# Optimization experiments

Hardware: AMD Instinct MI355X
Metric: run time of the kernel (lower is better)

The kernel has to match this reference:

```python
import jax, jax.numpy as jnp
from jax import lax
import numpy as np

DN = ('NCHW', 'OIHW', 'NCHW')

def _bn(x, g, b):
    # BatchNorm2d in training mode: batch statistics, biased variance, eps=1e-5
    m = jnp.mean(x, axis=(0, 2, 3), keepdims=True)
    v = jnp.var(x, axis=(0, 2, 3), keepdims=True)
    return g[None, :, None, None] * (x - m) * lax.rsqrt(v + 1e-5) + b[None, :, None, None]

def _conv(x, w, b, s, p):
    y = lax.conv_general_dilated(x, w, (s, s), [(p, p), (p, p)], dimension_numbers=DN)
    return y + b[None, :, None, None]

def _convt(x, w, b, s, p):
    # torch ConvTranspose2d weight layout [in, out, k, k]; equivalent to
    # input-dilated conv with flipped, transposed kernel and padding k-1-p.
    k = w.shape[2]
    pp = k - 1 - p
    w2 = jnp.flip(w, (2, 3)).transpose(1, 0, 2, 3)  # [out, in, k, k]
    y = lax.conv_general_dilated(x, w2, (1, 1), [(pp, pp), (pp, pp)],
                                 lhs_dilation=(s, s), dimension_numbers=DN)
    return y + b[None, :, None, None]

def setup_inputs() -> dict:
    key = jax.random.key(0)
    ks = jax.random.split(key, 16)
    f32 = jnp.float32
    def rn(i, shape, s):
        return jax.random.normal(ks[i], shape, f32) * s
    K = 256
    inp = {
        'x': jax.random.normal(ks[0], (128, 3, 64, 64), f32),
        'codebook': jax.random.uniform(ks[1], (256, 256), f32, -1.0 / K, 1.0 / K),
        'e_w1': rn(2, (64, 3, 3, 3), 0.19), 'e_b1': jnp.zeros((64,), f32),
        'e_g1': jnp.ones((64,), f32), 'e_be1': jnp.zeros((64,), f32),
        'e_w2': rn(3, (128, 64, 4, 4), 0.031), 'e_b2': jnp.zeros((128,), f32),
        'e_g2': jnp.ones((128,), f32), 'e_be2': jnp.zeros((128,), f32),
        'e_w3': rn(4, (192, 128, 4, 4), 0.022), 'e_b3': jnp.zeros((192,), f32),
        'e_g3': jnp.ones((192,), f32), 'e_be3': jnp.zeros((192,), f32),
        'e_w4': rn(5, (256, 192, 1, 1), 0.072), 'e_b4': jnp.zeros((256,), f32),
        'd_w1': rn(6, (256, 192, 1, 1), 0.062), 'd_b1': jnp.zeros((192,), f32),
        'd_g1': jnp.ones((192,), f32), 'd_be1': jnp.zeros((192,), f32),
        'd_w2': rn(7, (192, 128, 4, 4), 0.018), 'd_b2': jnp.zeros((128,), f32),
        'd_g2': jnp.ones((128,), f32), 'd_be2': jnp.zeros((128,), f32),
        'd_w3': rn(8, (128, 64, 4, 4), 0.022), 'd_b3': jnp.zeros((64,), f32),
        'd_g3': jnp.ones((64,), f32), 'd_be3': jnp.zeros((64,), f32),
        'd_w4': rn(9, (3, 64, 3, 3), 0.042), 'd_b4': jnp.zeros((3,), f32),
    }
    return inp

def reference(x, codebook,
              e_w1, e_b1, e_g1, e_be1, e_w2, e_b2, e_g2, e_be2,
              e_w3, e_b3, e_g3, e_be3, e_w4, e_b4,
              d_w1, d_b1, d_g1, d_be1, d_w2, d_b2, d_g2, d_be2,
              d_w3, d_b3, d_g3, d_be3, d_w4, d_b4):
    # encoder
    h = jax.nn.relu(_bn(_conv(x, e_w1, e_b1, 1, 1), e_g1, e_be1))
    h = jax.nn.relu(_bn(_conv(h, e_w2, e_b2, 2, 1), e_g2, e_be2))
    h = jax.nn.relu(_bn(_conv(h, e_w3, e_b3, 2, 1), e_g3, e_be3))
    h = _conv(h, e_w4, e_b4, 1, 0)  # [B, 256, 16, 16]
    B, C, H, W = h.shape
    Z = h.transpose(0, 2, 3, 1).reshape(-1, C)  # [N, D]
    # fused cdist via ||a||^2 + ||b||^2 - 2ab (argmin invariant to const offsets)
    d2 = (jnp.sum(Z * Z, axis=1, keepdims=True)
          + jnp.sum(codebook * codebook, axis=1)[None, :]
          - 2.0 * (Z @ codebook.T))  # [N, K]
    j = jnp.argmin(d2, axis=1)
    Wj = codebook[j]  # [N, D]
    loss_commit = jnp.mean(jnp.sum((Z - lax.stop_gradient(Wj)) ** 2, axis=1))
    loss_code = jnp.mean(jnp.sum((lax.stop_gradient(Z) - Wj) ** 2, axis=1))
    hq = Wj.reshape(B, H, W, C).transpose(0, 3, 1, 2)
    # decoder
    g = jax.nn.relu(_bn(_convt(hq, d_w1, d_b1, 1, 0), d_g1, d_be1))
    g = jax.nn.relu(_bn(_convt(g, d_w2, d_b2, 2, 1), d_g2, d_be2))
    g = jax.nn.relu(_bn(_convt(g, d_w3, d_b3, 2, 1), d_g3, d_be3))
    g = _conv(g, d_w4, d_b4, 1, 1)  # [B, 3, 64, 64]
    return g, loss_commit, loss_code
```

## Files before the change

kernel.cpp:

```cpp
#include <hip/hip_runtime.h>

#define TPB 256

typedef __attribute__((ext_vector_type(4))) float v4f;
typedef __attribute__((ext_vector_type(8))) short v8s;

__device__ __forceinline__ float us2f(unsigned int u) {
    union { unsigned int i; float f; } w; w.i = u << 16; return w.f;
}
__device__ __forceinline__ unsigned short f2us(float f) {
    union { float ff; unsigned int i; } w; w.ff = f;
    unsigned int u = w.i;
    return (unsigned short)((u + 0x7fffu + ((u >> 16) & 1u)) >> 16);
}
__device__ __forceinline__ void gl_lds16(const unsigned short* g, unsigned short* l) {
    __builtin_amdgcn_global_load_lds(
        (const __attribute__((address_space(1))) unsigned int*)g,
        (__attribute__((address_space(3))) unsigned int*)l, 16, 0, 0);
}

__global__ __launch_bounds__(TPB) void repack_all(
    const float* __restrict__ e_w1, const float* __restrict__ d_w4,
    const float* __restrict__ e_w2, const float* __restrict__ e_w3,
    const float* __restrict__ e_w4, const float* __restrict__ d_w1,
    const float* __restrict__ d_w2, const float* __restrict__ d_w3,
    unsigned short* __restrict__ we1, unsigned short* __restrict__ wd4r,
    unsigned short* __restrict__ we2, unsigned short* __restrict__ we3,
    unsigned short* __restrict__ we4, unsigned short* __restrict__ wd1,
    unsigned short* __restrict__ wd2, unsigned short* __restrict__ wd3,
    unsigned short* __restrict__ zpage)
{
    int gid = blockIdx.x * TPB + threadIdx.x;
    if (gid < 2048) {
        int idx = gid;
        int k = idx & 31, co = idx >> 5;
        we1[idx] = (k < 27) ? f2us(e_w1[co * 27 + k]) : (unsigned short)0;
        return;
    }
    gid -= 2048;
    if (gid < 9216) {
        int idx = gid;
        int e = idx & 7;
        int lane = (idx >> 3) & 63;
        int kk = idx >> 9;
        int lr = lane & 15, lc = lane >> 4;
        int tap = kk >> 1, half = kk & 1;
        int ci = half * 32 + lc * 8 + e;
        wd4r[idx] = (lr < 3) ? f2us(d_w4[((size_t)lr * 64 + ci) * 9 + tap])
                             : (unsigned short)0;
        return;
    }
    gid -= 9216;
    if (gid < 131072) {
        int idx = gid;
        int e = idx & 7;
        int lane = (idx >> 3) & 63;
        int seg8 = (idx >> 9) & 7;
        int u = idx >> 12;
        int cb = u % 2, tap = u / 2;
        int lr = lane & 15, lc = lane >> 4;
        int kc = seg8 >> 2, sg = seg8 & 3;
        int co = cb * 64 + sg * 16 + lr;
        int ci = kc * 32 + lc * 8 + e;
        we2[idx] = f2us(e_w2[((size_t)co * 64 + ci) * 16 + tap]);
        return;
    }
    gid -= 131072;
    if (gid < 393216) {
        int idx = gid;
        int ci = idx % 128;
        int co = (idx / 128) % 192;
        int kk = idx / (128 * 192);
        we3[idx] = f2us(e_w3[((size_t)co * 128 + ci) * 16 + kk]);
        return;
    }
    gid -= 393216;
    if (gid < 49152) {
        int idx = gid;
        int ci = idx % 192;
        int co = (idx / 192) % 256;
        we4[idx] = f2us(e_w4[(size_t)co * 192 + ci]);
        return;
    }
    gid -= 49152;
    if (gid < 49152) {
        int idx = gid;
        int ci = idx % 256;
        int co = idx / 256;
        wd1[idx] = f2us(d_w1[(size_t)ci * 192 + co]);
        return;
    }
    gid -= 49152;
    if (gid < 393216) {
        int idx = gid;
        int e = idx & 7;
        int lane = (idx >> 3) & 63;
        int seg8 = (idx >> 9) & 7;
        int u = idx >> 12;
        int cb = u % 2;
        int u2 = u / 2;
        int cc = u2 % 3;
        int tk = u2 / 3;
        int kidx = tk & 3, cls = tk >> 2;
        int lr = lane & 15, lc = lane >> 4;
        int kc = seg8 >> 2, sg = seg8 & 3;
        int co = cb * 64 + sg * 16 + lr;
        int ci = cc * 64 + kc * 32 + lc * 8 + e;
        int ohp = cls >> 1, owp = cls & 1;
        int kh = ((ohp + 1) & 1) + 2 * (kidx >> 1);
        int kw = ((owp + 1) & 1) + 2 * (kidx & 1);
        wd2[idx] = f2us(d_w2[((size_t)ci * 128 + co) * 16 + kh * 4 + kw]);
        return;
    }
    gid -= 393216;
    if (gid < 131072) {
        int idx = gid;
        int e = idx & 7;
        int lane = (idx >> 3) & 63;
        int seg8 = (idx >> 9) & 7;
        int u2 = idx >> 12;
        int cc = u2 % 2;
        int tk = u2 / 2;
        int kidx = tk & 3, cls = tk >> 2;
        int lr = lane & 15, lc = lane >> 4;
        int kc = seg8 >> 2, sg = seg8 & 3;
        int co = sg * 16 + lr;
        int ci = cc * 64 + kc * 32 + lc * 8 + e;
        int ohp = cls >> 1, owp = cls & 1;
        int kh = ((ohp + 1) & 1) + 2 * (kidx >> 1);
        int kw = ((owp + 1) & 1) + 2 * (kidx & 1);
        wd3[idx] = f2us(d_w3[((size_t)ci * 64 + co) * 16 + kh * 4 + kw]);
        return;
    }
    gid -= 131072;
    if (gid < 128) zpage[gid] = 0;
}

__global__ __launch_bounds__(TPB) void e1_gemm(
    const float* __restrict__ x, const unsigned short* __restrict__ wrep,
    const float* __restrict__ bias, unsigned short* __restrict__ yout,
    float* __restrict__ part, int N)
{
    __shared__ __align__(16) unsigned short Ab[8 * 512];
    __shared__ __align__(16) unsigned short Bb[4 * 512];

    const int t = threadIdx.x, lane = t & 63, wave = t >> 6;
    const int wm = wave >> 1, wn = wave & 1;
    const int m0 = (int)blockIdx.x * 128;
    const int lr = lane & 15, lc = lane >> 4;

    gl_lds16(wrep + (size_t)(wave * 16 + lr) * 32 + lc * 8, &Bb[wave * 512]);

    {
        int r = m0 + (t >> 1);
        int h = t & 1;
        int n = r >> 12, oh = (r >> 6) & 63, ow = r & 63;
        unsigned short rowv[16];
#pragma unroll
        for (int kk = 0; kk < 16; kk++) {
            int k = h * 16 + kk;
            float v = 0.f;
            if (k < 27) {
                int ci = k / 9, tap = k % 9, kh = tap / 3, kw = tap % 3;
                int ih = oh - 1 + kh, iw = ow - 1 + kw;
                if ((unsigned)ih < 64u && (unsigned)iw < 64u)
                    v = x[(((size_t)n * 3 + ci) * 64 + ih) * 64 + iw];
            }
            rowv[kk] = f2us(v);
        }
        int rl = (t >> 1) & 15;
        int s = (t >> 1) >> 4;
        int base = s * 512 + (h * 32 + rl) * 8;
        *(int4*)&Ab[base] = *(const int4*)&rowv[0];
        *(int4*)&Ab[base + 128] = *(const int4*)&rowv[8];
    }
    __syncthreads();

    v4f acc[4][2];
#pragma unroll
    for (int i = 0; i < 4; i++)
#pragma unroll
        for (int j = 0; j < 2; j++)
#pragma unroll
            for (int r = 0; r < 4; r++) acc[i][j][r] = 0.f;

    v8s a[4], b[2];
#pragma unroll
    for (int i = 0; i < 4; i++)
        a[i] = *(const v8s*)&Ab[(wm * 4 + i) * 512 + lane * 8];
#pragma unroll
    for (int j = 0; j < 2; j++)
        b[j] = *(const v8s*)&Bb[(wn * 2 + j) * 512 + lane * 8];
#pragma unroll
    for (int i = 0; i < 4; i++)
#pragma unroll
        for (int j = 0; j < 2; j++)
            acc[i][j] = __builtin_amdgcn_mfma_f32_16x16x32_bf16(a[i], b[j], acc[i][j], 0, 0, 0);

    float sloc[2], qloc[2];
#pragma unroll
    for (int j = 0; j < 2; j++) { sloc[j] = 0.f; qloc[j] = 0.f; }

#pragma unroll
    for (int i = 0; i < 4; i++) {
        int mr = wm * 64 + i * 16 + (lane >> 4) * 4;
#pragma unroll
        for (int j = 0; j < 2; j++) {
            int col = wn * 32 + j * 16 + (lane & 15);
            float bs = bias[col];
#pragma unroll
            for (int r = 0; r < 4; r++) {
                int row = m0 + mr + r;
                int n = row >> 12, oh = (row >> 6) & 63, ow = row & 63;
                int cls = ((oh & 1) << 1) | (ow & 1);
                size_t crow = ((((size_t)cls * N + n) * 32 + (oh >> 1)) * 32 + (ow >> 1));
                float v = acc[i][j][r] + bs;
                yout[crow * 64 + col] = f2us(v);
                sloc[j] += v;
                qloc[j] += v * v;
            }
        }
    }

    __syncthreads();
    float* red = (float*)Ab;
    for (int i = t; i < 128; i += TPB) red[i] = 0.f;
    __syncthreads();
#pragma unroll
    for (int j = 0; j < 2; j++) {
        float s = sloc[j], qv = qloc[j];
        s += __shfl_xor(s, 16); s += __shfl_xor(s, 32);
        qv += __shfl_xor(qv, 16); qv += __shfl_xor(qv, 32);
        if ((lane >> 4) == 0) {
            int cl = wn * 32 + j * 16 + (lane & 15);
            atomicAdd(&red[cl], s);
            atomicAdd(&red[64 + cl], qv);
        }
    }
    __syncthreads();
    int PB = (int)gridDim.x, pb = (int)blockIdx.x;
    for (int i = t; i < 64; i += TPB) {
        part[(size_t)i * PB + pb] = red[i];
        part[(size_t)(64 + i) * PB + pb] = red[64 + i];
    }
}

template<int CIN, int COUT, int HO, int WO, int NCB>
__global__ __launch_bounds__(TPB) void conv_c(
    const unsigned short* __restrict__ xin, const unsigned short* __restrict__ wrep,
    const float* __restrict__ bias, unsigned short* __restrict__ yout,
    float* __restrict__ part, const unsigned short* __restrict__ zpage, int N)
{
    constexpr int NCI = CIN / 64;
    constexpr int NIT = 16 * NCI;
    __shared__ __align__(16) unsigned short Ab[2][16 * 1024];
    __shared__ __align__(16) unsigned short Bb[2][8 * 512];

    const int t = threadIdx.x, lane = t & 63, wave = t >> 6;
    int gdec = (int)blockIdx.x >> 3, xs = (int)blockIdx.x & 7;
    int cb = 0;
    if (NCB >= 2) { cb = gdec % NCB; gdec /= NCB; }
    const int tile = (gdec << 3) + xs;
    const int m0 = tile * 256;
    const int co0 = cb * 64;
    const int lr = lane & 15, lc = lane >> 4;

    const int jr7 = lane >> 3;
    const int sw = ((lane & 7) ^ jr7) * 8;

    int n_[4], oh_[4], ow0_[4];
#pragma unroll
    for (int q = 0; q < 4; q++) {
        int r0 = m0 + (wave * 4 + q) * 16;
        n_[q] = r0 / (HO * WO);
        int rem = r0 % (HO * WO);
        oh_[q] = rem / WO;
        ow0_[q] = rem % WO;
    }

    v4f acc[4][4];
#pragma unroll
    for (int i = 0; i < 4; i++)
#pragma unroll
        for (int j = 0; j < 4; j++)
#pragma unroll
            for (int r = 0; r < 4; r++) acc[i][j][r] = 0.f;

    auto stage = [&](int it, int buf) {
        const int tap = it / NCI, cc = it % NCI;
        const int kh = tap >> 2, kw = tap & 3;
        const int dcls = (((kh + 1) & 1) << 1) | ((kw + 1) & 1);
        const int dh2 = (kh - 1) >> 1;
        const int dw2 = (kw - 1) >> 1;
#pragma unroll
        for (int q = 0; q < 4; q++) {
            const int ih2 = oh_[q] + dh2;
            const bool ihv = (unsigned)ih2 < (unsigned)HO;
#pragma unroll
            for (int h = 0; h < 2; h++) {
                int iw2 = ow0_[q] + h * 8 + jr7 + dw2;
                bool av = ihv && (unsigned)iw2 < (unsigned)WO;
                size_t ab = ((((size_t)dcls * N + n_[q]) * HO + ih2) * WO + iw2) * CIN;
                const unsigned short* src = av ? xin + ab + cc * 64 + sw : zpage;
                gl_lds16(src, &Ab[buf][(wave * 4 + q) * 1024 + h * 512]);
            }
        }
        const unsigned short* wb = wrep
            + ((size_t)(tap * NCI + cc) * NCB + cb) * 4096;
        gl_lds16(wb + wave * 512 + lane * 8, &Bb[buf][wave * 512]);
        gl_lds16(wb + (4 + wave) * 512 + lane * 8, &Bb[buf][(4 + wave) * 512]);
    };

    auto compute = [&](int it, int buf) {
#pragma unroll
        for (int kc = 0; kc < 2; kc++) {
            v8s a[4], b[4];
#pragma unroll
            for (int i = 0; i < 4; i++)
                a[i] = *(const v8s*)&Ab[buf][(wave * 4 + i) * 1024 + lr * 64
                        + ((kc * 32 + lc * 8) ^ ((lr & 7) << 3))];
#pragma unroll
            for (int j = 0; j < 4; j++)
                b[j] = *(const v8s*)&Bb[buf][(kc * 4 + j) * 512 + lane * 8];
#pragma unroll
            for (int i = 0; i < 4; i++)
#pragma unroll
                for (int j = 0; j < 4; j++)
                    acc[i][j] = __builtin_amdgcn_mfma_f32_16x16x32_bf16(a[i], b[j], acc[i][j], 0, 0, 0);
        }
    };

    stage(0, 0);
    __syncthreads();

#pragma unroll
    for (int it = 0; it < NIT; ++it) {
        const int buf = it & 1;
        if (it + 1 < NIT) stage(it + 1, buf ^ 1);
        compute(it, buf);
        __syncthreads();
    }

    float sloc[4], qloc[4];
#pragma unroll
    for (int j = 0; j < 4; j++) { sloc[j] = 0.f; qloc[j] = 0.f; }

#pragma unroll
    for (int i = 0; i < 4; i++) {
        int mr = wave * 64 + i * 16 + (lane >> 4) * 4;
#pragma unroll
        for (int j = 0; j < 4; j++) {
            int col = co0 + j * 16 + (lane & 15);
            float bs = bias[col];
#pragma unroll
            for (int r = 0; r < 4; r++) {
                size_t gi = (size_t)(m0 + mr + r) * COUT + col;
                float v = acc[i][j][r] + bs;
                yout[gi] = f2us(v);
                sloc[j] += v;
                qloc[j] += v * v;
            }
        }
    }

    float* red = (float*)Ab;
    for (int i = t; i < 128; i += TPB) red[i] = 0.f;
    __syncthreads();
#pragma unroll
    for (int j = 0; j < 4; j++) {
        float s = sloc[j], qv = qloc[j];
        s += __shfl_xor(s, 16); s += __shfl_xor(s, 32);
        qv += __shfl_xor(qv, 16); qv += __shfl_xor(qv, 32);
        if ((lane >> 4) == 0) {
            int cl = j * 16 + (lane & 15);
            atomicAdd(&red[cl], s);
            atomicAdd(&red[64 + cl], qv);
        }
    }
    __syncthreads();
    const int TILES = (N * HO * WO) >> 8;
    const int pb = tile;
    for (int i = t; i < 64; i += TPB) {
        part[(size_t)(co0 + i) * TILES + pb] = red[i];
        part[(size_t)(COUT + co0 + i) * TILES + pb] = red[64 + i];
    }
}

template<int CIN, int COUT, int HIN, int WIN, int K, int S, int P, int BN,
         int OUTM, int NYB>
__global__ __launch_bounds__(TPB) void conv_mfma(
    const unsigned short* __restrict__ xin, const unsigned short* __restrict__ wrep,
    const float* __restrict__ bias, void* __restrict__ yout, void* __restrict__ yout2,
    float* __restrict__ part, const unsigned short* __restrict__ zpage, int N)
{
    constexpr int HOUT = (HIN + 2 * P - K) / S + 1;
    constexpr int WOUT = (WIN + 2 * P - K) / S + 1;
    constexpr int RN = BN / 32;
    constexpr int BSEG = BN / 16;
    constexpr int NCI = CIN / 64;
    constexpr int NIT = K * K * NCI;
    __shared__ __align__(16) unsigned short Ab[2][16 * 512];
    __shared__ __align__(16) unsigned short Bb[2][2 * BSEG * 512];

    const int t = threadIdx.x, lane = t & 63, wave = t >> 6;
    const int wm = wave >> 1, wn = wave & 1;
    int m0, co0;
    if (NYB == 2) {
        int g = (int)blockIdx.x >> 3, xs = (int)blockIdx.x & 7;
        co0 = (g & 1) * BN;
        m0 = (((g >> 1) << 3) + xs) * 128;
    } else {
        m0 = (int)blockIdx.x * 128;
        co0 = 0;
    }
    const int lr = lane & 15, lc = lane >> 4;

    int n_[2], oh_[2], ow_[2];
#pragma unroll
    for (int i = 0; i < 2; i++) {
        int r = m0 + (wave + 4 * i) * 16 + lr;
        n_[i] = r / (HOUT * WOUT);
        int rem = r % (HOUT * WOUT);
        oh_[i] = rem / WOUT;
        ow_[i] = rem % WOUT;
    }

    v4f acc[4][RN];
#pragma unroll
    for (int i = 0; i < 4; i++)
#pragma unroll
        for (int j = 0; j < RN; j++)
#pragma unroll
            for (int r = 0; r < 4; r++) acc[i][j][r] = 0.f;

    auto do_stage = [&](int it, int pb) {
        const int kk = it / NCI;
        const int ci0 = (it % NCI) * 64;
        const int kh = kk / K, kw = kk % K;
#pragma unroll
        for (int i = 0; i < 2; i++) {
            int ih = oh_[i] * S - P + kh;
            int iw = ow_[i] * S - P + kw;
            bool av = (unsigned)ih < (unsigned)HIN && (unsigned)iw < (unsigned)WIN;
            const unsigned short* b0 = av
                ? xin + (((size_t)n_[i] * HIN + ih) * WIN + iw) * CIN + lc * 8 + ci0
                : zpage;
            gl_lds16(b0, &Ab[pb][(wave + 4 * i) * 512]);
            gl_lds16(av ? b0 + 32 : zpage, &Ab[pb][(8 + wave + 4 * i) * 512]);
        }
        const unsigned short* wt = wrep + (size_t)kk * COUT * CIN;
#pragma unroll
        for (int i = 0; i < 2; i++) {
            int sgb = wave + 4 * i;
            if (sgb < BSEG) {
                const unsigned short* wb =
                    wt + (size_t)(co0 + sgb * 16 + lr) * CIN + ci0 + lc * 8;
                gl_lds16(wb, &Bb[pb][sgb * 512]);
                gl_lds16(wb + 32, &Bb[pb][(BSEG + sgb) * 512]);
            }
        }
    };

    do_stage(0, 0);
    __syncthreads();

    for (int it = 0; it < NIT; ++it) {
        const int pb = it & 1;
        if (it + 1 < NIT) do_stage(it + 1, pb ^ 1);

#pragma unroll
        for (int kc = 0; kc < 2; kc++) {
            v8s a[4], b[RN];
#pragma unroll
            for (int i = 0; i < 4; i++)
                a[i] = *(const v8s*)&Ab[pb][(kc * 8 + wm * 4 + i) * 512 + lane * 8];
#pragma unroll
            for (int j = 0; j < RN; j++)
                b[j] = *(const v8s*)&Bb[pb][(kc * BSEG + wn * RN + j) * 512 + lane * 8];
#pragma unroll
            for (int i = 0; i < 4; i++)
#pragma unroll
                for (int j = 0; j < RN; j++)
                    acc[i][j] = __builtin_amdgcn_mfma_f32_16x16x32_bf16(a[i], b[j], acc[i][j], 0, 0, 0);
        }
        __syncthreads();
    }

    float sloc[RN], qloc[RN];
#pragma unroll
    for (int j = 0; j < RN; j++) { sloc[j] = 0.f; qloc[j] = 0.f; }

#pragma unroll
    for (int i = 0; i < 4; i++) {
        int mr = wm * 64 + i * 16 + (lane >> 4) * 4;
#pragma unroll
        for (int j = 0; j < RN; j++) {
            int col = co0 + wn * (BN / 2) + j * 16 + (lane & 15);
            float bs = bias[col];
#pragma unroll
            for (int r = 0; r < 4; r++) {
                size_t g = (size_t)(m0 + mr + r) * COUT + col;
                float v = acc[i][j][r] + bs;
                if (OUTM == 2) {
                    unsigned short h = f2us(v);
                    ((unsigned short*)yout)[g] = h;
                    ((unsigned short*)yout2)[g] = f2us(v - us2f(h));
                } else {
                    ((unsigned short*)yout)[g] = f2us(v);
                    sloc[j] += v;
                    qloc[j] += v * v;
                }
            }
        }
    }

    if (OUTM == 0) {
        __syncthreads();
        float* red = (float*)Ab;
        for (int i = t; i < 2 * BN; i += TPB) red[i] = 0.f;
        __syncthreads();
#pragma unroll
        for (int j = 0; j < RN; j++) {
            float s = sloc[j], qv = qloc[j];
            s += __shfl_xor(s, 16); s += __shfl_xor(s, 32);
            qv += __shfl_xor(qv, 16); qv += __shfl_xor(qv, 32);
            if ((lane >> 4) == 0) {
                int cl = wn * (BN / 2) + j * 16 + (lane & 15);
                atomicAdd(&red[cl], s);
                atomicAdd(&red[BN + cl], qv);
            }
        }
        __syncthreads();
        int pb = (NYB == 2) ? (m0 >> 7) : (int)blockIdx.x;
        int PB = (NYB == 2) ? ((int)gridDim.x >> 1) : (int)gridDim.x;
        for (int i = t; i < BN; i += TPB) {
            int col = co0 + i;
            part[(size_t)col * PB + pb] = red[i];
            part[(size_t)(COUT + col) * PB + pb] = red[BN + i];
        }
    }
}

template<int CIN, int COUT, int HIN, int WIN, int NCB, int IN_CLS>
__global__ __launch_bounds__(TPB) void convt_c(
    const unsigned short* __restrict__ xin, const unsigned short* __restrict__ wrep,
    const float* __restrict__ bias, unsigned short* __restrict__ yout,
    float* __restrict__ part, const unsigned short* __restrict__ zpage, int N)
{
    constexpr int NCI = CIN / 64;
    constexpr int NIT = 4 * NCI;
    __shared__ __align__(16) unsigned short Ab[2][16 * 1024];
    __shared__ __align__(16) unsigned short Bb[2][8 * 512];

    const int t = threadIdx.x, lane = t & 63, wave = t >> 6;
    int gdec = (int)blockIdx.x >> 3, xs = (int)blockIdx.x & 7;
    int cb = 0;
    if (NCB == 2) { cb = gdec & 1; gdec >>= 1; }
    const int cls = gdec & 3;
    const int tile = ((gdec >> 2) << 3) + xs;
    const int m0 = tile * 256;
    const int co0 = cb * 64;
    const int ohp = cls >> 1, owp = cls & 1;
    const int khb = (ohp + 1) & 1, kwb = (owp + 1) & 1;
    const int dh0 = (ohp + 1 - khb) >> 1, dw0 = (owp + 1 - kwb) >> 1;
    const int lr = lane & 15, lc = lane >> 4;

    const int jr7 = lane >> 3;
    const int sw = ((lane & 7) ^ jr7) * 8;

    int n_[4], i_[4], j0_[4];
#pragma unroll
    for (int q = 0; q < 4; q++) {
        int r0 = m0 + (wave * 4 + q) * 16;
        n_[q] = r0 / (HIN * WIN);
        int rem = r0 % (HIN * WIN);
        i_[q] = rem / WIN;
        j0_[q] = rem % WIN;
    }

    v4f acc[4][4];
#pragma unroll
    for (int i = 0; i < 4; i++)
#pragma unroll
        for (int j = 0; j < 4; j++)
#pragma unroll
            for (int r = 0; r < 4; r++) acc[i][j][r] = 0.f;

    auto stage = [&](int it, int buf) {
        const int tap = it / NCI, cc = it % NCI;
        const int dh = dh0 - (tap >> 1);
        const int dw = dw0 - (tap & 1);
#pragma unroll
        for (int q = 0; q < 4; q++) {
            const int ih = i_[q] + dh;
            const bool ihv = (unsigned)ih < (unsigned)HIN;
#pragma unroll
            for (int h = 0; h < 2; h++) {
                int iw = j0_[q] + h * 8 + jr7 + dw;
                bool av = ihv && (unsigned)iw < (unsigned)WIN;
                size_t ab;
                if (IN_CLS) {
                    int clsi = ((ih & 1) << 1) | (iw & 1);
                    ab = ((((size_t)clsi * N + n_[q]) * (HIN / 2) + (ih >> 1)) * (WIN / 2)
                         + (iw >> 1)) * CIN;
                } else {
                    ab = (((size_t)n_[q] * HIN + ih) * WIN + iw) * CIN;
                }
                const unsigned short* src = av ? xin + ab + cc * 64 + sw : zpage;
                gl_lds16(src, &Ab[buf][(wave * 4 + q) * 1024 + h * 512]);
            }
        }
        const unsigned short* wb = wrep
            + ((size_t)((cls * 4 + tap) * NCI + cc) * NCB + cb) * 4096;
        gl_lds16(wb + wave * 512 + lane * 8, &Bb[buf][wave * 512]);
        gl_lds16(wb + (4 + wave) * 512 + lane * 8, &Bb[buf][(4 + wave) * 512]);
    };

    auto compute = [&](int it, int buf) {
#pragma unroll
        for (int kc = 0; kc < 2; kc++) {
            v8s a[4], b[4];
#pragma unroll
            for (int i = 0; i < 4; i++)
                a[i] = *(const v8s*)&Ab[buf][(wave * 4 + i) * 1024 + lr * 64
                        + ((kc * 32 + lc * 8) ^ ((lr & 7) << 3))];
#pragma unroll
            for (int j = 0; j < 4; j++)
                b[j] = *(const v8s*)&Bb[buf][(kc * 4 + j) * 512 + lane * 8];
#pragma unroll
            for (int i = 0; i < 4; i++)
#pragma unroll
                for (int j = 0; j < 4; j++)
                    acc[i][j] = __builtin_amdgcn_mfma_f32_16x16x32_bf16(a[i], b[j], acc[i][j], 0, 0, 0);
        }
    };

    stage(0, 0);
    __syncthreads();

#pragma unroll
    for (int it = 0; it < NIT; ++it) {
        const int buf = it & 1;
        if (it + 1 < NIT) stage(it + 1, buf ^ 1);
        compute(it, buf);
        __syncthreads();
    }

    float sloc[4], qloc[4];
#pragma unroll
    for (int j = 0; j < 4; j++) { sloc[j] = 0.f; qloc[j] = 0.f; }

    const size_t clsbase = (size_t)cls * N * HIN * WIN;
#pragma unroll
    for (int i = 0; i < 4; i++) {
        int mr = wave * 64 + i * 16 + (lane >> 4) * 4;
#pragma unroll
        for (int j = 0; j < 4; j++) {
            int col = co0 + j * 16 + (lane & 15);
            float bs = bias[col];
#pragma unroll
            for (int r = 0; r < 4; r++) {
                size_t gi = (clsbase + m0 + mr + r) * COUT + col;
                float v = acc[i][j][r] + bs;
                yout[gi] = f2us(v);
                sloc[j] += v;
                qloc[j] += v * v;
            }
        }
    }

    float* red = (float*)Ab;
    for (int i = t; i < 128; i += TPB) red[i] = 0.f;
    __syncthreads();
#pragma unroll
    for (int j = 0; j < 4; j++) {
        float s = sloc[j], qv = qloc[j];
        s += __shfl_xor(s, 16); s += __shfl_xor(s, 32);
        qv += __shfl_xor(qv, 16); qv += __shfl_xor(qv, 32);
        if ((lane >> 4) == 0) {
            int cl = j * 16 + (lane & 15);
            atomicAdd(&red[cl], s);
            atomicAdd(&red[64 + cl], qv);
        }
    }
    __syncthreads();
    const int TILES = (N * HIN * WIN) >> 8;
    const int PB = 4 * TILES;
    const int pb = cls * TILES + tile;
    for (int i = t; i < 64; i += TPB) {
        part[(size_t)(co0 + i) * PB + pb] = red[i];
        part[(size_t)(COUT + co0 + i) * PB + pb] = red[64 + i];
    }
}

template<int C>
__global__ __launch_bounds__(64) void bn_reduce2(
    const float* __restrict__ part, float* __restrict__ st, int B)
{
    int i = blockIdx.x;
    int lane = threadIdx.x;
    float s = 0.f;
    for (int b = lane; b < B; b += 64) s += part[(size_t)i * B + b];
#pragma unroll
    for (int off = 1; off < 64; off <<= 1) s += __shfl_xor(s, off);
    if (lane == 0) st[i] = s;
}

template<int C>
__global__ __launch_bounds__(TPB) void bn_apply_v(
    unsigned short* __restrict__ x, const float* __restrict__ st,
    const float* __restrict__ g, const float* __restrict__ be, int M)
{
    __shared__ float sc[C], sh[C];
    int t = threadIdx.x;
    float cnt = (float)M;
    for (int c = t; c < C; c += TPB) {
        float m = st[c] / cnt;
        float v = st[C + c] / cnt - m * m;
        float s = g[c] * rsqrtf(v + 1e-5f);
        sc[c] = s;
        sh[c] = be[c] - m * s;
    }
    __syncthreads();
    constexpr int GPT = C / 8;
    size_t tot = (size_t)M * GPT;
    for (size_t slot = (size_t)blockIdx.x * TPB + t; slot < tot;
         slot += (size_t)gridDim.x * TPB) {
        int c0 = (int)(slot % GPT) * 8;
        int4 v = *(int4*)(x + slot * 8);
        unsigned int* vu = (unsigned int*)&v;
#pragma unroll
        for (int k = 0; k < 4; k++) {
            float f0 = fmaxf(us2f(vu[k] & 0xffffu) * sc[c0 + 2 * k] + sh[c0 + 2 * k], 0.f);
            float f1 = fmaxf(us2f(vu[k] >> 16) * sc[c0 + 2 * k + 1] + sh[c0 + 2 * k + 1], 0.f);
            vu[k] = (unsigned int)f2us(f0) | ((unsigned int)f2us(f1) << 16);
        }
        *(int4*)(x + slot * 8) = v;
    }
}

__global__ __launch_bounds__(TPB) void cb_prep(
    const float* __restrict__ cb, unsigned short* __restrict__ chb,
    unsigned short* __restrict__ clb, float* __restrict__ cn2)
{
    int j = blockIdx.x, d = threadIdx.x;
    float v = cb[j * 256 + d];
    unsigned short h = f2us(v);
    chb[j * 256 + d] = h;
    clb[j * 256 + d] = f2us(v - us2f(h));
    float s = v * v;
#pragma unroll
    for (int off = 1; off < 64; off <<= 1) s += __shfl_xor(s, off);
    __shared__ float p[4];
    if ((d & 63) == 0) p[d >> 6] = s;
    __syncthreads();
    if (d == 0) cn2[j] = p[0] + p[1] + p[2] + p[3];
}

__global__ __launch_bounds__(TPB) void vq_gemm(
    const unsigned short* __restrict__ zh, const unsigned short* __restrict__ zl,
    const unsigned short* __restrict__ chb, const unsigned short* __restrict__ clb,
    const float* __restrict__ cn2, float* __restrict__ valp, int* __restrict__ idxp)
{
    __shared__ __align__(16) unsigned short Ah[2][8 * 512];
    __shared__ __align__(16) unsigned short Al[2][8 * 512];
    __shared__ __align__(16) unsigned short Bh[2][8 * 512];
    __shared__ __align__(16) unsigned short Bl[2][8 * 512];

    const int t = threadIdx.x, lane = t & 63, wave = t >> 6;
    const int wm = wave >> 1, wn = wave & 1;
    const int gdec = (int)blockIdx.x >> 3, xs = (int)blockIdx.x & 7;
    const int cbk = gdec & 1;
    const int m0 = (((gdec >> 1) << 3) + xs) * 128;
    const int co0 = cbk * 128;
    const int lr = lane & 15, lc = lane >> 4;

    size_t a0 = (size_t)(m0 + wave * 16 + lr) * 256 + lc * 8;
    size_t a1 = a0 + 64 * 256;
    size_t b0 = (size_t)(co0 + wave * 16 + lr) * 256 + lc * 8;
    size_t b1 = b0 + 64 * 256;

    v4f acc[4][4];
#pragma unroll
    for (int i = 0; i < 4; i++)
#pragma unroll
        for (int j = 0; j < 4; j++)
#pragma unroll
            for (int r = 0; r < 4; r++) acc[i][j][r] = 0.f;

    auto do_stage = [&](int ci0, int pb) {
        gl_lds16(zh + a0 + ci0, &Ah[pb][wave * 512]);
        gl_lds16(zh + a1 + ci0, &Ah[pb][(wave + 4) * 512]);
        gl_lds16(zl + a0 + ci0, &Al[pb][wave * 512]);
        gl_lds16(zl + a1 + ci0, &Al[pb][(wave + 4) * 512]);
        gl_lds16(chb + b0 + ci0, &Bh[pb][wave * 512]);
        gl_lds16(chb + b1 + ci0, &Bh[pb][(wave + 4) * 512]);
        gl_lds16(clb + b0 + ci0, &Bl[pb][wave * 512]);
        gl_lds16(clb + b1 + ci0, &Bl[pb][(wave + 4) * 512]);
    };

    do_stage(0, 0);
    __syncthreads();

    for (int s = 0; s < 8; ++s) {
        const int pb = s & 1;
        if (s < 7) do_stage((s + 1) * 32, pb ^ 1);

        v8s a_h[4], a_l[4], b_h[4], b_l[4];
#pragma unroll
        for (int i = 0; i < 4; i++) {
            a_h[i] = *(const v8s*)&Ah[pb][(wm * 4 + i) * 512 + lane * 8];
            a_l[i] = *(const v8s*)&Al[pb][(wm * 4 + i) * 512 + lane * 8];
        }
#pragma unroll
        for (int j = 0; j < 4; j++) {
            b_h[j] = *(const v8s*)&Bh[pb][(wn * 4 + j) * 512 + lane * 8];
            b_l[j] = *(const v8s*)&Bl[pb][(wn * 4 + j) * 512 + lane * 8];
        }
#pragma unroll
        for (int i = 0; i < 4; i++)
#pragma unroll
            for (int j = 0; j < 4; j++) {
                acc[i][j] = __builtin_amdgcn_mfma_f32_16x16x32_bf16(a_h[i], b_h[j], acc[i][j], 0, 0, 0);
                acc[i][j] = __builtin_amdgcn_mfma_f32_16x16x32_bf16(a_h[i], b_l[j], acc[i][j], 0, 0, 0);
                acc[i][j] = __builtin_amdgcn_mfma_f32_16x16x32_bf16(a_l[i], b_h[j], acc[i][j], 0, 0, 0);
            }
        __syncthreads();
    }

#pragma unroll
    for (int i = 0; i < 4; i++) {
#pragma unroll
        for (int r = 0; r < 4; r++) {
            float best = 3.4e38f;
            int bi = 0;
#pragma unroll
            for (int j = 0; j < 4; j++) {
                int col = co0 + wn * 64 + j * 16 + (lane & 15);
                float d = cn2[col] - 2.f * acc[i][j][r];
                if (d < best || (d == best && col < bi)) { best = d; bi = col; }
            }
#pragma unroll
            for (int off = 1; off < 16; off <<= 1) {
                float ov = __shfl_xor(best, off);
                int oi = __shfl_xor(bi, off);
                if (ov < best || (ov == best && oi < bi)) { best = ov; bi = oi; }
            }
            if ((lane & 15) == 0) {
                int row = m0 + wm * 64 + i * 16 + (lane >> 4) * 4 + r;
                valp[(size_t)row * 4 + cbk * 2 + wn] = best;
                idxp[(size_t)row * 4 + cbk * 2 + wn] = bi;
            }
        }
    }
}

__global__ __launch_bounds__(TPB) void vq_gather2(
    const unsigned short* __restrict__ zh, const unsigned short* __restrict__ zl,
    const float* __restrict__ cb, const float* __restrict__ valp,
    const int* __restrict__ idxp, unsigned short* __restrict__ hq,
    float* __restrict__ rowloss)
{
    int row = blockIdx.x * 4 + (threadIdx.x >> 6);
    int lane = threadIdx.x & 63;
    float best = valp[(size_t)row * 4];
    int j = idxp[(size_t)row * 4];
#pragma unroll
    for (int c = 1; c < 4; c++) {
        float v = valp[(size_t)row * 4 + c];
        if (v < best) { best = v; j = idxp[(size_t)row * 4 + c]; }
    }
    ushort4 hv = *(const ushort4*)(zh + (size_t)row * 256 + lane * 4);
    ushort4 lv = *(const ushort4*)(zl + (size_t)row * 256 + lane * 4);
    float4 cv = *(const float4*)(cb + (size_t)j * 256 + lane * 4);
    float z0 = us2f(hv.x) + us2f(lv.x);
    float z1 = us2f(hv.y) + us2f(lv.y);
    float z2 = us2f(hv.z) + us2f(lv.z);
    float z3 = us2f(hv.w) + us2f(lv.w);
    float d0 = z0 - cv.x, d1 = z1 - cv.y, d2 = z2 - cv.z, d3 = z3 - cv.w;
    float d = d0 * d0 + d1 * d1 + d2 * d2 + d3 * d3;
#pragma unroll
    for (int off = 1; off < 64; off <<= 1) d += __shfl_xor(d, off);
    if (lane == 0) rowloss[row] = d;
    ushort4 o;
    o.x = f2us(cv.x); o.y = f2us(cv.y); o.z = f2us(cv.z); o.w = f2us(cv.w);
    *(ushort4*)(hq + (size_t)row * 256 + lane * 4) = o;
}

__global__ __launch_bounds__(TPB) void loss_all(
    const float* __restrict__ rowloss, float* __restrict__ out2)
{
    int t = threadIdx.x;
    float v = 0.f;
    for (int i = t; i < 32768; i += TPB) v += rowloss[i];
#pragma unroll
    for (int off = 1; off < 64; off <<= 1) v += __shfl_xor(v, off);
    __shared__ float p[4];
    if ((t & 63) == 0) p[t >> 6] = v;
    __syncthreads();
    if (t == 0) {
        float m = (p[0] + p[1] + p[2] + p[3]) * (1.0f / 32768.0f);
        out2[0] = m;
        out2[1] = m;
    }
}

__global__ __launch_bounds__(TPB) void conv_d4(
    const unsigned short* __restrict__ xb, const unsigned short* __restrict__ wrep,
    const float* __restrict__ st, const float* __restrict__ gg,
    const float* __restrict__ be, const float* __restrict__ bias,
    float* __restrict__ out, int N)
{
    __shared__ __align__(16) unsigned short xsm[8 * 409 * 8];
    __shared__ float scs[64], shs[64];
    int4* xsI = (int4*)xsm;
    const int t = threadIdx.x;
    const int lane = t & 63, wave = t >> 6;
    const int lr = lane & 15, lc = lane >> 4;

    if (t < 64) {
        float cnt = (float)(N * 4096);
        float m = st[t] / cnt;
        float vv = st[64 + t] / cnt - m * m;
        float s = gg[t] * rsqrtf(vv + 1e-5f);
        scs[t] = s;
        shs[t] = be[t] - m * s;
    }
    __syncthreads();

    const int n = blockIdx.x >> 4;
    const int tile = blockIdx.x & 15;
    const int th = tile >> 2, tw = tile & 3;
    const int ihh0 = 8 * th - 1, iwh0 = 8 * tw - 1;

    for (int s = t; s < 3200; s += TPB) {
        int cls = s / 800;
        int rem = s % 800;
        int ihh_l = rem / 80;
        int i4 = rem % 80;
        int iwh_l = i4 >> 3, c8 = i4 & 7;
        int ihh_g = ihh0 + ihh_l;
        int iwh_g = iwh0 + iwh_l;
        int4 v;
        if ((unsigned)ihh_g < 32u && (unsigned)iwh_g < 32u) {
            size_t row = (((size_t)cls * 128 + n) * 32 + ihh_g) * 32 + iwh_g;
            v = *(const int4*)(xb + row * 64 + c8 * 8);
            unsigned int* vu = (unsigned int*)&v;
            int c0 = c8 * 8;
#pragma unroll
            for (int k = 0; k < 4; k++) {
                float f0 = fmaxf(us2f(vu[k] & 0xffffu) * scs[c0 + 2 * k] + shs[c0 + 2 * k], 0.f);
                float f1 = fmaxf(us2f(vu[k] >> 16) * scs[c0 + 2 * k + 1] + shs[c0 + 2 * k + 1], 0.f);
                vu[k] = (unsigned int)f2us(f0) | ((unsigned int)f2us(f1) << 16);
            }
        } else {
            v.x = v.y = v.z = v.w = 0;
        }
        xsI[c8 * 409 + cls * 102 + ihh_l * 10 + iwh_l] = v;
    }
    __syncthreads();

    int abase[4][9];
#pragma unroll
    for (int q = 0; q < 4; q++) {
        int seg = wave * 4 + q;
        int oh = th * 16 + seg;
        int ow = tw * 16 + lr;
#pragma unroll
        for (int tap = 0; tap < 9; tap++) {
            int kh = tap / 3, kw = tap % 3;
            int ih = oh - 1 + kh, iw = ow - 1 + kw;
            int clsi = ((ih & 1) << 1) | (iw & 1);
            abase[q][tap] = clsi * 102 + ((ih >> 1) - ihh0) * 10 + ((iw >> 1) - iwh0);
        }
    }

    v4f acc[4];
#pragma unroll
    for (int q = 0; q < 4; q++)
#pragma unroll
        for (int r = 0; r < 4; r++) acc[q][r] = 0.f;

#pragma unroll
    for (int kk = 0; kk < 18; kk++) {
        const int tap = kk >> 1, half = kk & 1;
        const int c8 = half * 4 + lc;
        v8s b = *(const v8s*)(wrep + kk * 512 + lane * 8);
#pragma unroll
        for (int q = 0; q < 4; q++) {
            v8s a = *(const v8s*)&xsI[c8 * 409 + abase[q][tap]];
            acc[q] = __builtin_amdgcn_mfma_f32_16x16x32_bf16(a, b, acc[q], 0, 0, 0);
        }
    }

    if (lr < 3) {
        float bs = bias[lr];
#pragma unroll
        for (int q = 0; q < 4; q++) {
            int seg = wave * 4 + q;
            int oh = th * 16 + seg;
            int ow0 = tw * 16 + lc * 4;
            float4 v;
            v.x = acc[q][0] + bs; v.y = acc[q][1] + bs;
            v.z = acc[q][2] + bs; v.w = acc[q][3] + bs;
            *(float4*)&out[((size_t)n * 3 + lr) * 4096 + oh * 64 + ow0] = v;
        }
    }
}


extern "C" void kernel_launch(void* const* d_in, const int* in_sizes, int n_in,
                              void* d_out, int out_size, void* d_ws, size_t ws_size,
                              hipStream_t stream) {
    const float* x    = (const float*)d_in[0];
    const float* cb   = (const float*)d_in[1];
    const float* e_w1 = (const float*)d_in[2];  const float* e_b1 = (const float*)d_in[3];
    const float* e_g1 = (const float*)d_in[4];  const float* e_be1 = (const float*)d_in[5];
    const float* e_w2 = (const float*)d_in[6];  const float* e_b2 = (const float*)d_in[7];
    const float* e_g2 = (const float*)d_in[8];  const float* e_be2 = (const float*)d_in[9];
    const float* e_w3 = (const float*)d_in[10]; const float* e_b3 = (const float*)d_in[11];
    const float* e_g3 = (const float*)d_in[12]; const float* e_be3 = (const float*)d_in[13];
    const float* e_w4 = (const float*)d_in[14]; const float* e_b4 = (const float*)d_in[15];
    const float* d_w1 = (const float*)d_in[16]; const float* d_b1 = (const float*)d_in[17];
    const float* d_g1 = (const float*)d_in[18]; const float* d_be1 = (const float*)d_in[19];
    const float* d_w2 = (const float*)d_in[20]; const float* d_b2 = (const float*)d_in[21];
    const float* d_g2 = (const float*)d_in[22]; const float* d_be2 = (const float*)d_in[23];
    const float* d_w3 = (const float*)d_in[24]; const float* d_b3 = (const float*)d_in[25];
    const float* d_g3 = (const float*)d_in[26]; const float* d_be3 = (const float*)d_in[27];
    const float* d_w4 = (const float*)d_in[28]; const float* d_b4 = (const float*)d_in[29];

    float* ws = (float*)d_ws;
    unsigned short* h1 = (unsigned short*)(ws);
    unsigned short* g3 = h1;
    unsigned short* h2 = (unsigned short*)(ws + 16777216);
    unsigned short* g2 = h2;
    unsigned short* h3 = (unsigned short*)(ws + 25165824);
    unsigned short* g1 = h3;
    unsigned short* zh = (unsigned short*)(ws + 28311552);
    unsigned short* zl = (unsigned short*)(ws + 32505856);
    unsigned short* hq = (unsigned short*)(ws + 36700160);
    float* stats = ws + 40960000;
    unsigned short* we1 = (unsigned short*)(ws + 40963072);
    unsigned short* wd4r = (unsigned short*)(ws + 40964096);
    float* cn2 = ws + 40995904;
    unsigned short* chb = (unsigned short*)(ws + 40996160);
    unsigned short* clb = (unsigned short*)(ws + 41028928);
    unsigned short* wrep = (unsigned short*)(ws + 41061696);
    unsigned short* we2 = wrep + 0;
    unsigned short* we3 = wrep + 131072;
    unsigned short* we4 = wrep + 524288;
    unsigned short* wd1 = wrep + 573440;
    unsigned short* wd2 = wrep + 622592;
    unsigned short* wd3 = wrep + 1015808;
    float* part = ws + 41635136;
    float* valp = part;
    int* idxp = (int*)(part + 131072);
    float* rowloss = ws + 50023744;
    unsigned short* zpage = (unsigned short*)(ws + 50122112);
    float* out = (float*)d_out;
    float* losses = out + 1572864;

    const int N = 128;

    repack_all<<<4525, TPB, 0, stream>>>(
        e_w1, d_w4, e_w2, e_w3, e_w4, d_w1, d_w2, d_w3,
        we1, wd4r, we2, we3, we4, wd1, wd2, wd3, zpage);
    cb_prep<<<256, TPB, 0, stream>>>(cb, chb, clb, cn2);

    e1_gemm<<<4096, TPB, 0, stream>>>(x, we1, e_b1, h1, part, N);
    bn_reduce2<64><<<128, 64, 0, stream>>>(part, stats + 0 * 512, 4096);
    bn_apply_v<64><<<4096, TPB, 0, stream>>>(h1, stats + 0 * 512, e_g1, e_be1, 524288);

    conv_c<64, 128, 32, 32, 2>
        <<<1024, TPB, 0, stream>>>(h1, we2, e_b2, h2, part, zpage, N);
    bn_reduce2<128><<<256, 64, 0, stream>>>(part, stats + 1 * 512, 512);
    bn_apply_v<128><<<2048, TPB, 0, stream>>>(h2, stats + 1 * 512, e_g2, e_be2, 131072);

    conv_mfma<128, 192, 32, 32, 4, 2, 1, 96, 0, 2>
        <<<512, TPB, 0, stream>>>(h2, we3, e_b3, h3, nullptr, part, zpage, N);
    bn_reduce2<192><<<384, 64, 0, stream>>>(part, stats + 2 * 512, 256);
    bn_apply_v<192><<<1024, TPB, 0, stream>>>(h3, stats + 2 * 512, e_g3, e_be3, 32768);

    conv_mfma<192, 256, 16, 16, 1, 1, 0, 128, 2, 2>
        <<<512, TPB, 0, stream>>>(h3, we4, e_b4, zh, zl, nullptr, zpage, N);

    vq_gemm<<<512, TPB, 0, stream>>>(zh, zl, chb, clb, cn2, valp, idxp);
    vq_gather2<<<8192, TPB, 0, stream>>>(zh, zl, cb, valp, idxp, hq, rowloss);
    loss_all<<<1, TPB, 0, stream>>>(rowloss, losses);

    conv_mfma<256, 192, 16, 16, 1, 1, 0, 96, 0, 2>
        <<<512, TPB, 0, stream>>>(hq, wd1, d_b1, g1, nullptr, part, zpage, N);
    bn_reduce2<192><<<384, 64, 0, stream>>>(part, stats + 3 * 512, 256);
    bn_apply_v<192><<<1024, TPB, 0, stream>>>(g1, stats + 3 * 512, d_g1, d_be1, 32768);

    convt_c<192, 128, 16, 16, 2, 0>
        <<<1024, TPB, 0, stream>>>(g1, wd2, d_b2, g2, part, zpage, N);
    bn_reduce2<128><<<256, 64, 0, stream>>>(part, stats + 4 * 512, 512);
    bn_apply_v<128><<<2048, TPB, 0, stream>>>(g2, stats + 4 * 512, d_g2, d_be2, 131072);

    convt_c<128, 64, 32, 32, 1, 1>
        <<<2048, TPB, 0, stream>>>(g2, wd3, d_b3, g3, part, zpage, N);
    bn_reduce2<64><<<128, 64, 0, stream>>>(part, stats + 5 * 512, 2048);

    conv_d4<<<2048, TPB, 0, stream>>>(g3, wd4r, stats + 5 * 512, d_g3, d_be3,
                                      d_b4, out, N);
}
```

Baseline: 572.9 us.

## Add double-buffered transposed-conv kernel with register-held B for COUT=64 layer

Adds a specialised transposed-conv kernel for the last decoder upsampling layer (COUT=64). It stages A tiles into LDS with global_load_lds in a two-deep ping-pong and loads weight fragments straight into registers rather than through shared memory. Waits use explicit vmcnt/lgkmcnt counts so loads can overlap the MFMA work. This removes LDS traffic for B and some synchronisation, at the cost of more registers per thread and fragile hand-tuned wait counts.

```diff
diff --git a/kernel.cpp b/kernel.cpp
--- a/kernel.cpp
+++ b/kernel.cpp
@@ -690,6 +690,161 @@
     for (int i = t; i < 64; i += TPB) {
         part[(size_t)(co0 + i) * PB + pb] = red[i];
         part[(size_t)(COUT + co0 + i) * PB + pb] = red[64 + i];
+    }
+}
+
+template<int CIN, int COUT, int HIN, int WIN, int IN_CLS>
+__global__ __launch_bounds__(TPB) void convt_nb(
+    const unsigned short* __restrict__ xin, const unsigned short* __restrict__ wrep,
+    const float* __restrict__ bias, unsigned short* __restrict__ yout,
+    float* __restrict__ part, const unsigned short* __restrict__ zpage, int N)
+{
+    constexpr int NCI = CIN / 64;
+    constexpr int NIT = 4 * NCI;
+    __shared__ __align__(16) unsigned short Ab[2][16 * 1024];
+    __shared__ float red[128];
+
+    const int t = threadIdx.x, lane = t & 63, wave = t >> 6;
+    int gdec = (int)blockIdx.x >> 3, xs = (int)blockIdx.x & 7;
+    const int cls = gdec & 3;
+    const int tile = ((gdec >> 2) << 3) + xs;
+    const int m0 = tile * 256;
+    const int ohp = cls >> 1, owp = cls & 1;
+    const int khb = (ohp + 1) & 1, kwb = (owp + 1) & 1;
+    const int dh0 = (ohp + 1 - khb) >> 1, dw0 = (owp + 1 - kwb) >> 1;
+    const int lr = lane & 15, lc = lane >> 4;
+
+    const int jr7 = lane >> 3;
+    const int sw = ((lane & 7) ^ jr7) * 8;
+
+    int n_[4], i_[4], j0_[4];
+#pragma unroll
+    for (int q = 0; q < 4; q++) {
+        int r0 = m0 + (wave * 4 + q) * 16;
+        n_[q] = r0 / (HIN * WIN);
+        int rem = r0 % (HIN * WIN);
+        i_[q] = rem / WIN;
+        j0_[q] = rem % WIN;
+    }
+
+    v4f acc[4][4];
+#pragma unroll
+    for (int i = 0; i < 4; i++)
+#pragma unroll
+        for (int j = 0; j < 4; j++)
+#pragma unroll
+            for (int r = 0; r < 4; r++) acc[i][j][r] = 0.f;
+
+    auto stageA = [&](int it, int buf) {
+        const int tap = it / NCI, cc = it % NCI;
+        const int dh = dh0 - (tap >> 1);
+        const int dw = dw0 - (tap & 1);
+#pragma unroll
+        for (int q = 0; q < 4; q++) {
+            const int ih = i_[q] + dh;
+            const bool ihv = (unsigned)ih < (unsigned)HIN;
+#pragma unroll
+            for (int h = 0; h < 2; h++) {
+                int iw = j0_[q] + h * 8 + jr7 + dw;
+                bool av = ihv && (unsigned)iw < (unsigned)WIN;
+                size_t ab;
+                if (IN_CLS) {
+                    int clsi = ((ih & 1) << 1) | (iw & 1);
+                    ab = ((((size_t)clsi * N + n_[q]) * (HIN / 2) + (ih >> 1)) * (WIN / 2)
+                         + (iw >> 1)) * CIN;
+                } else {
+                    ab = (((size_t)n_[q] * HIN + ih) * WIN + iw) * CIN;
+                }
+                const unsigned short* src = av ? xin + ab + cc * 64 + sw : zpage;
+                gl_lds16(src, &Ab[buf][(wave * 4 + q) * 1024 + h * 512]);
+            }
+        }
+    };
+    auto loadB = [&](int it, v8s (&breg)[8]) {
+        const int tap = it / NCI, cc = it % NCI;
+        const unsigned short* wb = wrep + (size_t)((cls * 4 + tap) * NCI + cc) * 4096;
+#pragma unroll
+        for (int s = 0; s < 8; s++)
+            breg[s] = *(const v8s*)(wb + s * 512 + lane * 8);
+    };
+    auto computeIt = [&](int buf, const v8s (&breg)[8]) {
+#pragma unroll
+        for (int kc = 0; kc < 2; kc++) {
+            v8s a[4];
+#pragma unroll
+            for (int i = 0; i < 4; i++)
+                a[i] = *(const v8s*)&Ab[buf][(wave * 4 + i) * 1024 + lr * 64
+                        + ((kc * 32 + lc * 8) ^ ((lr & 7) << 3))];
+#pragma unroll
+            for (int i = 0; i < 4; i++)
+#pragma unroll
+                for (int j = 0; j < 4; j++)
+                    acc[i][j] = __builtin_amdgcn_mfma_f32_16x16x32_bf16(a[i], breg[kc * 4 + j], acc[i][j], 0, 0, 0);
+        }
+    };
+
+    v8s bA[8], bB[8];
+    stageA(0, 0); loadB(0, bA);
+    stageA(1, 1); loadB(1, bB);
+
+#pragma unroll
+    for (int it = 0; it < NIT; ++it) {
+        const int buf = it & 1;
+        if (it + 1 < NIT) { asm volatile("s_waitcnt vmcnt(16)" ::: "memory"); }
+        else              { asm volatile("s_waitcnt vmcnt(0)" ::: "memory"); }
+        __builtin_amdgcn_sched_barrier(0);
+        if (buf == 0) computeIt(0, bA); else computeIt(1, bB);
+        if (it + 2 < NIT) {
+            asm volatile("s_waitcnt lgkmcnt(0)" ::: "memory");
+            __builtin_amdgcn_sched_barrier(0);
+            stageA(it + 2, buf);
+            if (buf == 0) loadB(it + 2, bA); else loadB(it + 2, bB);
+        }
+    }
+
+    float sloc[4], qloc[4];
+#pragma unroll
+    for (int j = 0; j < 4; j++) { sloc[j] = 0.f; qloc[j] = 0.f; }
+
+    const size_t clsbase = (size_t)cls * N * HIN * WIN;
+#pragma unroll
+    for (int i = 0; i < 4; i++) {
+        int mr = wave * 64 + i * 16 + (lane >> 4) * 4;
+#pragma unroll
+        for (int j = 0; j < 4; j++) {
+            int col = j * 16 + (lane & 15);
+            float bs = bias[col];
+#pragma unroll
+            for (int r = 0; r < 4; r++) {
+                size_t gi = (clsbase + m0 + mr + r) * COUT + col;
+                float v = acc[i][j][r] + bs;
+                yout[gi] = f2us(v);
+                sloc[j] += v;
+                qloc[j] += v * v;
+            }
+        }
+    }
+
+    for (int i = t; i < 128; i += TPB) red[i] = 0.f;
+    __syncthreads();
+#pragma unroll
+    for (int j = 0; j < 4; j++) {
+        float s = sloc[j], qv = qloc[j];
+        s += __shfl_xor(s, 16); s += __shfl_xor(s, 32);
+        qv += __shfl_xor(qv, 16); qv += __shfl_xor(qv, 32);
+        if ((lane >> 4) == 0) {
+            int cl = j * 16 + (lane & 15);
+            atomicAdd(&red[cl], s);
+            atomicAdd(&red[64 + cl], qv);
+        }
+    }
+    __syncthreads();
+    const int TILES = (N * HIN * WIN) >> 8;
+    const int PB = 4 * TILES;
+    const int pb = cls * TILES + tile;
+    for (int i = t; i < 64; i += TPB) {
+        part[(size_t)i * PB + pb] = red[i];
+        part[(size_t)(COUT + i) * PB + pb] = red[64 + i];
     }
 }
 
@@ -1098,7 +1253,7 @@
     bn_reduce2<128><<<256, 64, 0, stream>>>(part, stats + 4 * 512, 512);
     bn_apply_v<128><<<2048, TPB, 0, stream>>>(g2, stats + 4 * 512, d_g2, d_be2, 131072);
 
-    convt_c<128, 64, 32, 32, 1, 1>
+    convt_nb<128, 64, 32, 32, 1>
         <<<2048, TPB, 0, stream>>>(g2, wd3, d_b3, g3, part, zpage, N);
     bn_reduce2<64><<<128, 64, 0, stream>>>(part, stats + 5 * 512, 2048);
 
```

New measurement: 572.1 us. Within noise of the previous version (-0.1%).

## Restructure transposed-conv main loop: B in registers, barrier-free prefetch, precomputed offsets

Applied to the files above, without the earlier changes.

The transposed-conv kernel now loads weight fragments straight into registers instead of staging them through LDS. It precomputes per-tap byte offsets for the A gathers once, outside the loop. The main loop prefetches two iterations ahead and uses explicit vmcnt/lgkmcnt waits in place of block-wide __syncthreads. This is meant to cut LDS traffic, address arithmetic and barrier stalls, at the cost of more VGPRs and reliance on hand-counted wait values. The zero page is also enlarged so that column-offset reads from it stay in bounds.

```diff
diff --git a/kernel.cpp b/kernel.cpp
--- a/kernel.cpp
+++ b/kernel.cpp
@@ -133,7 +133,7 @@
         return;
     }
     gid -= 131072;
-    if (gid < 128) zpage[gid] = 0;
+    if (gid < 256) zpage[gid] = 0;
 }
 
 __global__ __launch_bounds__(TPB) void e1_gemm(
@@ -542,7 +542,7 @@
 }
 
 template<int CIN, int COUT, int HIN, int WIN, int NCB, int IN_CLS>
-__global__ __launch_bounds__(TPB) void convt_c(
+__global__ __launch_bounds__(TPB) void convt_nb(
     const unsigned short* __restrict__ xin, const unsigned short* __restrict__ wrep,
     const float* __restrict__ bias, unsigned short* __restrict__ yout,
     float* __restrict__ part, const unsigned short* __restrict__ zpage, int N)
@@ -550,7 +550,7 @@
     constexpr int NCI = CIN / 64;
     constexpr int NIT = 4 * NCI;
     __shared__ __align__(16) unsigned short Ab[2][16 * 1024];
-    __shared__ __align__(16) unsigned short Bb[2][8 * 512];
+    __shared__ float red[128];
 
     const int t = threadIdx.x, lane = t & 63, wave = t >> 6;
     int gdec = (int)blockIdx.x >> 3, xs = (int)blockIdx.x & 7;
@@ -578,6 +578,35 @@
         j0_[q] = rem % WIN;
     }
 
+    int aoffb[4][4][2];
+    {
+        const int zdb = (int)((const char*)zpage - (const char*)xin);
+#pragma unroll
+        for (int q = 0; q < 4; q++) {
+#pragma unroll
+            for (int tap = 0; tap < 4; tap++) {
+                const int dh = dh0 - (tap >> 1);
+                const int dw = dw0 - (tap & 1);
+                const int ih = i_[q] + dh;
+                const bool ihv = (unsigned)ih < (unsigned)HIN;
+#pragma unroll
+                for (int h = 0; h < 2; h++) {
+                    int iw = j0_[q] + h * 8 + jr7 + dw;
+                    bool av = ihv && (unsigned)iw < (unsigned)WIN;
+                    size_t ab;
+                    if (IN_CLS) {
+                        int clsi = ((ih & 1) << 1) | (iw & 1);
+                        ab = ((((size_t)clsi * N + n_[q]) * (HIN / 2) + (ih >> 1)) * (WIN / 2)
+                             + (iw >> 1)) * CIN;
+                    } else {
+                        ab = (((size_t)n_[q] * HIN + ih) * WIN + iw) * CIN;
+                    }
+                    aoffb[q][tap][h] = av ? (int)((ab + sw) * 2) : zdb;
+                }
+            }
+        }
+    }
+
     v4f acc[4][4];
 #pragma unroll
     for (int i = 0; i < 4; i++)
@@ -586,64 +615,59 @@
 #pragma unroll
             for (int r = 0; r < 4; r++) acc[i][j][r] = 0.f;
 
-    auto stage = [&](int it, int buf) {
+    auto stageA = [&](int it, int buf) {
         const int tap = it / NCI, cc = it % NCI;
-        const int dh = dh0 - (tap >> 1);
-        const int dw = dw0 - (tap & 1);
 #pragma unroll
         for (int q = 0; q < 4; q++) {
-            const int ih = i_[q] + dh;
-            const bool ihv = (unsigned)ih < (unsigned)HIN;
 #pragma unroll
             for (int h = 0; h < 2; h++) {
-                int iw = j0_[q] + h * 8 + jr7 + dw;
-                bool av = ihv && (unsigned)iw < (unsigned)WIN;
-                size_t ab;
-                if (IN_CLS) {
-                    int clsi = ((ih & 1) << 1) | (iw & 1);
-                    ab = ((((size_t)clsi * N + n_[q]) * (HIN / 2) + (ih >> 1)) * (WIN / 2)
-                         + (iw >> 1)) * CIN;
-                } else {
-                    ab = (((size_t)n_[q] * HIN + ih) * WIN + iw) * CIN;
-                }
-                const unsigned short* src = av ? xin + ab + cc * 64 + sw : zpage;
+                const unsigned short* src = (const unsigned short*)
+                    ((const char*)xin + aoffb[q][tap][h] + cc * 128);
                 gl_lds16(src, &Ab[buf][(wave * 4 + q) * 1024 + h * 512]);
             }
         }
+    };
+    auto loadB = [&](int it, v8s (&breg)[8]) {
+        const int tap = it / NCI, cc = it % NCI;
         const unsigned short* wb = wrep
             + ((size_t)((cls * 4 + tap) * NCI + cc) * NCB + cb) * 4096;
-        gl_lds16(wb + wave * 512 + lane * 8, &Bb[buf][wave * 512]);
-        gl_lds16(wb + (4 + wave) * 512 + lane * 8, &Bb[buf][(4 + wave) * 512]);
+#pragma unroll
+        for (int s = 0; s < 8; s++)
+            breg[s] = *(const v8s*)(wb + s * 512 + lane * 8);
     };
-
-    auto compute = [&](int it, int buf) {
+    auto computeIt = [&](int buf, const v8s (&breg)[8]) {
 #pragma unroll
         for (int kc = 0; kc < 2; kc++) {
-            v8s a[4], b[4];
+            v8s a[4];
 #pragma unroll
             for (int i = 0; i < 4; i++)
                 a[i] = *(const v8s*)&Ab[buf][(wave * 4 + i) * 1024 + lr * 64
                         + ((kc * 32 + lc * 8) ^ ((lr & 7) << 3))];
 #pragma unroll
-            for (int j = 0; j < 4; j++)
-                b[j] = *(const v8s*)&Bb[buf][(kc * 4 + j) * 512 + lane * 8];
-#pragma unroll
             for (int i = 0; i < 4; i++)
 #pragma unroll
                 for (int j = 0; j < 4; j++)
-                    acc[i][j] = __builtin_amdgcn_mfma_f32_16x16x32_bf16(a[i], b[j], acc[i][j], 0, 0, 0);
+                    acc[i][j] = __builtin_amdgcn_mfma_f32_16x16x32_bf16(a[i], breg[kc * 4 + j], acc[i][j], 0, 0, 0);
         }
     };
 
-    stage(0, 0);
-    __syncthreads();
+    v8s bA[8], bB[8];
+    stageA(0, 0); loadB(0, bA);
+    stageA(1, 1); loadB(1, bB);
 
 #pragma unroll
     for (int it = 0; it < NIT; ++it) {
         const int buf = it & 1;
-        if (it + 1 < NIT) stage(it + 1, buf ^ 1);
-        compute(it, buf);
-        __syncthreads();
+        if (it + 1 < NIT) { asm volatile("s_waitcnt vmcnt(16)" ::: "memory"); }
+        else              { asm volatile("s_waitcnt vmcnt(0)" ::: "memory"); }
+        __builtin_amdgcn_sched_barrier(0);
+        if (buf == 0) computeIt(0, bA); else computeIt(1, bB);
+        if (it + 2 < NIT) {
+            asm volatile("s_waitcnt lgkmcnt(0)" ::: "memory");
+            __builtin_amdgcn_sched_barrier(0);
+            stageA(it + 2, buf);
+            if (buf == 0) loadB(it + 2, bA); else loadB(it + 2, bB);
+        }
     }
 
     float sloc[4], qloc[4];
@@ -669,7 +693,6 @@
         }
     }
 
-    float* red = (float*)Ab;
     for (int i = t; i < 128; i += TPB) red[i] = 0.f;
     __syncthreads();
 #pragma unroll
@@ -1093,12 +1116,12 @@
     bn_reduce2<192><<<384, 64, 0, stream>>>(part, stats + 3 * 512, 256);
     bn_apply_v<192><<<1024, TPB, 0, stream>>>(g1, stats + 3 * 512, d_g1, d_be1, 32768);
 
-    convt_c<192, 128, 16, 16, 2, 0>
+    convt_nb<192, 128, 16, 16, 2, 0>
         <<<1024, TPB, 0, stream>>>(g1, wd2, d_b2, g2, part, zpage, N);
     bn_reduce2<128><<<256, 64, 0, stream>>>(part, stats + 4 * 512, 512);
     bn_apply_v<128><<<2048, TPB, 0, stream>>>(g2, stats + 4 * 512, d_g2, d_be2, 131072);
 
-    convt_c<128, 64, 32, 32, 1, 1>
+    convt_nb<128, 64, 32, 32, 1, 1>
         <<<2048, TPB, 0, stream>>>(g2, wd3, d_b3, g3, part, zpage, N);
     bn_reduce2<64><<<128, 64, 0, stream>>>(part, stats + 5 * 512, 2048);
 
```

New measurement: 561.2 us. 1.02x faster.
